# Performance work log

Measured on AMD Instinct MI355X. Metric: run time of the kernel, lower is better.

Reference implementation:

```python
import jax, jax.numpy as jnp
import numpy as np


def setup_inputs() -> dict:
    key = jax.random.key(0)
    k1, k2, k3, k4 = jax.random.split(key, 4)
    H = W = 1024
    B = 16
    image = jax.random.normal(k1, (1, H, W), dtype=jnp.float32)
    x = jax.random.normal(k2, (B, 1, H, W), dtype=jnp.float32)
    # Conv2d(1, 9, 3) parameters, torch layout: weight (out=9, in=1, 3, 3), bias (9,)
    fan_in = 1 * 3 * 3
    bound = 1.0 / np.sqrt(fan_in)
    W_KL = jax.random.uniform(k3, (9, 1, 3, 3), jnp.float32, -bound, bound)
    b_KL = jax.random.uniform(k4, (9,), jnp.float32, -bound, bound)
    return {"image": image, "x": x, "W_KL": W_KL, "b_KL": b_KL}


def reference(image, x, W_KL, b_KL):
    # K = Conv2d(image): (1,H,W) -> (9,H,W), 'same' padding
    K = jax.lax.conv_general_dilated(
        image[None], W_KL, window_strides=(1, 1), padding='SAME',
        dimension_numbers=('NCHW', 'OIHW', 'NCHW'))[0] + b_KL[:, None, None]
    H, W = image.shape[1], image.shape[2]
    # permute (9,H,W) -> (H,W,9) -> unflatten to per-pixel 3x3 kernels (H,W,3,3)
    K = jnp.transpose(K, (1, 2, 0)).reshape(H, W, 3, 3)
    # Apply spatially-varying 3x3 kernel: y[b,c,h,w] = sum_{a,d} K[h,w,a,d] * x_pad[b,c,h+a,w+d]
    x_pad = jnp.pad(x, ((0, 0), (0, 0), (1, 1), (1, 1)))
    y = jnp.zeros_like(x)
    for a in range(3):
        for d in range(3):
            y = y + K[:, :, a, d] * x_pad[:, :, a:a + H, d:d + W]
    return y
```

## Files before the change

kernel.cpp:

```cpp
#include <hip/hip_runtime.h>

#define IH 1024
#define IW 1024
#define NB 16

__global__ __launch_bounds__(512) void fused_smblock(
    const float* __restrict__ image,
    const float* __restrict__ x,
    const float* __restrict__ Wk,
    const float* __restrict__ bk,
    float* __restrict__ out)
{
    const int tx = threadIdx.x;
    const int ty = threadIdx.y;
    const int w0 = blockIdx.x * 256 + tx * 4;
    const int h  = blockIdx.y * 8 + ty;

    float wk[81];
#pragma unroll
    for (int i = 0; i < 81; ++i) wk[i] = Wk[i];
    float bb[9];
#pragma unroll
    for (int c = 0; c < 9; ++c) bb[c] = bk[c];

    float p[3][6];
#pragma unroll
    for (int a = 0; a < 3; ++a) {
        const int hh = h + a - 1;
        if (hh >= 0 && hh < IH) {
            const float* row = image + (size_t)hh * IW;
            p[a][0] = (w0 > 0) ? row[w0 - 1] : 0.f;
            const float4 m = *(const float4*)(row + w0);
            p[a][1] = m.x; p[a][2] = m.y; p[a][3] = m.z; p[a][4] = m.w;
            p[a][5] = (w0 + 4 < IW) ? row[w0 + 4] : 0.f;
        } else {
#pragma unroll
            for (int j = 0; j < 6; ++j) p[a][j] = 0.f;
        }
    }

    float Kv[4][9];
#pragma unroll
    for (int j = 0; j < 4; ++j) {
#pragma unroll
        for (int c = 0; c < 9; ++c) {
            float acc = bb[c];
#pragma unroll
            for (int i = 0; i < 3; ++i)
#pragma unroll
                for (int jj = 0; jj < 3; ++jj)
                    acc = fmaf(wk[c * 9 + i * 3 + jj], p[i][j + jj], acc);
            Kv[j][c] = acc;
        }
    }

    const size_t plane = (size_t)IH * IW;
#pragma unroll 2
    for (int b = 0; b < NB; ++b) {
        const float* xp = x + (size_t)b * plane;
        float r[3][6];
#pragma unroll
        for (int a = 0; a < 3; ++a) {
            const int hh = h + a - 1;
            if (hh >= 0 && hh < IH) {
                const float* row = xp + (size_t)hh * IW;
                r[a][0] = (w0 > 0) ? row[w0 - 1] : 0.f;
                const float4 m = *(const float4*)(row + w0);
                r[a][1] = m.x; r[a][2] = m.y; r[a][3] = m.z; r[a][4] = m.w;
                r[a][5] = (w0 + 4 < IW) ? row[w0 + 4] : 0.f;
            } else {
#pragma unroll
                for (int j = 0; j < 6; ++j) r[a][j] = 0.f;
            }
        }
        float yv[4];
#pragma unroll
        for (int j = 0; j < 4; ++j) {
            float acc = 0.f;
#pragma unroll
            for (int a = 0; a < 3; ++a)
#pragma unroll
                for (int d = 0; d < 3; ++d)
                    acc = fmaf(Kv[j][a * 3 + d], r[a][j + d], acc);
            yv[j] = acc;
        }
        *(float4*)(out + (size_t)b * plane + (size_t)h * IW + w0) =
            make_float4(yv[0], yv[1], yv[2], yv[3]);
    }
}

extern "C" void kernel_launch(void* const* d_in, const int* in_sizes, int n_in,
                              void* d_out, int out_size, void* d_ws, size_t ws_size,
                              hipStream_t stream) {
    const float* image = (const float*)d_in[0];
    const float* x     = (const float*)d_in[1];
    const float* Wk    = (const float*)d_in[2];
    const float* bk    = (const float*)d_in[3];
    float* out = (float*)d_out;

    dim3 block(64, 8);
    dim3 grid(IW / 256, IH / 8);
    fused_smblock<<<grid, block, 0, stream>>>(image, x, Wk, bk, out);
}
```

Measured before the change: 147.3 us.

## Split batch across grid z, use wave shuffles for halos, nontemporal stores

The batch loop is split across a third grid dimension so each block handles four batch planes instead of sixteen. This gives four times as many blocks to fill the GPU, at the cost of recomputing the per-pixel kernel from the image four times. Left and right halo values now come from neighbouring lanes through wave shuffles rather than separate scalar global loads, with only the wave-edge lanes still loading from memory. Output stores are marked nontemporal to reduce cache pollution from the streamed result.

```diff
diff --git a/kernel.cpp b/kernel.cpp
--- a/kernel.cpp
+++ b/kernel.cpp
@@ -3,6 +3,24 @@
 #define IH 1024
 #define IW 1024
 #define NB 16
+#define BPB 4
+
+typedef float v4f __attribute__((ext_vector_type(4)));
+
+__device__ __forceinline__ void load_row6(const float* __restrict__ row, int w0,
+                                          int tx, bool valid, float o[6]) {
+    if (valid) {
+        const v4f m = *(const v4f*)(row + w0);
+        float left  = __shfl_up(m.w, 1);
+        float right = __shfl_down(m.x, 1);
+        if (tx == 0)  left  = (w0 > 0)      ? row[w0 - 1] : 0.f;
+        if (tx == 63) right = (w0 + 4 < IW) ? row[w0 + 4] : 0.f;
+        o[0] = left; o[1] = m.x; o[2] = m.y; o[3] = m.z; o[4] = m.w; o[5] = right;
+    } else {
+#pragma unroll
+        for (int j = 0; j < 6; ++j) o[j] = 0.f;
+    }
+}
 
 __global__ __launch_bounds__(512) void fused_smblock(
     const float* __restrict__ image,
@@ -27,16 +45,8 @@
 #pragma unroll
     for (int a = 0; a < 3; ++a) {
         const int hh = h + a - 1;
-        if (hh >= 0 && hh < IH) {
-            const float* row = image + (size_t)hh * IW;
-            p[a][0] = (w0 > 0) ? row[w0 - 1] : 0.f;
-            const float4 m = *(const float4*)(row + w0);
-            p[a][1] = m.x; p[a][2] = m.y; p[a][3] = m.z; p[a][4] = m.w;
-            p[a][5] = (w0 + 4 < IW) ? row[w0 + 4] : 0.f;
-        } else {
-#pragma unroll
-            for (int j = 0; j < 6; ++j) p[a][j] = 0.f;
-        }
+        load_row6(image + (size_t)(hh < 0 ? 0 : hh) * IW, w0, tx,
+                  (hh >= 0 && hh < IH), p[a]);
     }
 
     float Kv[4][9];
@@ -55,23 +65,16 @@
     }
 
     const size_t plane = (size_t)IH * IW;
+    const int b0 = blockIdx.z * BPB;
 #pragma unroll 2
-    for (int b = 0; b < NB; ++b) {
-        const float* xp = x + (size_t)b * plane;
+    for (int bi = 0; bi < BPB; ++bi) {
+        const float* xp = x + (size_t)(b0 + bi) * plane;
         float r[3][6];
 #pragma unroll
         for (int a = 0; a < 3; ++a) {
             const int hh = h + a - 1;
-            if (hh >= 0 && hh < IH) {
-                const float* row = xp + (size_t)hh * IW;
-                r[a][0] = (w0 > 0) ? row[w0 - 1] : 0.f;
-                const float4 m = *(const float4*)(row + w0);
-                r[a][1] = m.x; r[a][2] = m.y; r[a][3] = m.z; r[a][4] = m.w;
-                r[a][5] = (w0 + 4 < IW) ? row[w0 + 4] : 0.f;
-            } else {
-#pragma unroll
-                for (int j = 0; j < 6; ++j) r[a][j] = 0.f;
-            }
+            load_row6(xp + (size_t)(hh < 0 ? 0 : hh) * IW, w0, tx,
+                      (hh >= 0 && hh < IH), r[a]);
         }
         float yv[4];
 #pragma unroll
@@ -84,8 +87,9 @@
                     acc = fmaf(Kv[j][a * 3 + d], r[a][j + d], acc);
             yv[j] = acc;
         }
-        *(float4*)(out + (size_t)b * plane + (size_t)h * IW + w0) =
-            make_float4(yv[0], yv[1], yv[2], yv[3]);
+        v4f yvec; yvec.x = yv[0]; yvec.y = yv[1]; yvec.z = yv[2]; yvec.w = yv[3];
+        __builtin_nontemporal_store(
+            yvec, (v4f*)(out + (size_t)(b0 + bi) * plane + (size_t)h * IW + w0));
     }
 }
 
@@ -99,6 +103,6 @@
     float* out = (float*)d_out;
 
     dim3 block(64, 8);
-    dim3 grid(IW / 256, IH / 8);
+    dim3 grid(IW / 256, IH / 8, NB / BPB);
     fused_smblock<<<grid, block, 0, stream>>>(image, x, Wk, bk, out);
 }
```

Result: no change. 148.0 us (+0.4%).

## Double-buffer batch window loads, use branchless vector loads and nontemporal stores

Applied to the files above, without the earlier changes.

Prefetches the 3x6 input window for the next batch plane into a second register buffer while computing the current one, so load latency overlaps with FMAs. Halo loads become branchless aligned float2/float4 loads with clamped addresses and select-based zeroing. Output stores use a nontemporal hint, and the block shrinks from 64x8 to 64x4 threads with launch bounds 256. The double buffer raises register pressure, which may cut occupancy, and the extra halo loads pull in more bytes per thread.

```diff
diff --git a/kernel.cpp b/kernel.cpp
--- a/kernel.cpp
+++ b/kernel.cpp
@@ -4,7 +4,31 @@
 #define IW 1024
 #define NB 16
 
-__global__ __launch_bounds__(512) void fused_smblock(
+typedef float v4f __attribute__((ext_vector_type(4)));
+typedef float v2f __attribute__((ext_vector_type(2)));
+
+__device__ __forceinline__ void load_win(const float* __restrict__ plane,
+                                         int h, int w0, float win[3][6]) {
+#pragma unroll
+    for (int a = 0; a < 3; ++a) {
+        const int hh = h + a - 1;
+        const bool rowok = (hh >= 0) & (hh < IH);
+        const float* rowp = plane + (size_t)(rowok ? hh : 0) * IW;
+        const v2f lv = *(const v2f*)(rowp + (w0 > 0 ? w0 - 2 : 0));
+        const v4f mv = *(const v4f*)(rowp + w0);
+        const v2f rv = *(const v2f*)(rowp + (w0 + 4 < IW ? w0 + 4 : IW - 2));
+        const float fl = (rowok && w0 > 0)       ? lv.y : 0.f;
+        const float fr = (rowok && w0 + 4 < IW)  ? rv.x : 0.f;
+        win[a][0] = fl;
+        win[a][1] = rowok ? mv.x : 0.f;
+        win[a][2] = rowok ? mv.y : 0.f;
+        win[a][3] = rowok ? mv.z : 0.f;
+        win[a][4] = rowok ? mv.w : 0.f;
+        win[a][5] = fr;
+    }
+}
+
+__global__ __launch_bounds__(256) void fused_smblock(
     const float* __restrict__ image,
     const float* __restrict__ x,
     const float* __restrict__ Wk,
@@ -14,7 +38,7 @@
     const int tx = threadIdx.x;
     const int ty = threadIdx.y;
     const int w0 = blockIdx.x * 256 + tx * 4;
-    const int h  = blockIdx.y * 8 + ty;
+    const int h  = blockIdx.y * 4 + ty;
 
     float wk[81];
 #pragma unroll
@@ -24,56 +48,32 @@
     for (int c = 0; c < 9; ++c) bb[c] = bk[c];
 
     float p[3][6];
-#pragma unroll
-    for (int a = 0; a < 3; ++a) {
-        const int hh = h + a - 1;
-        if (hh >= 0 && hh < IH) {
-            const float* row = image + (size_t)hh * IW;
-            p[a][0] = (w0 > 0) ? row[w0 - 1] : 0.f;
-            const float4 m = *(const float4*)(row + w0);
-            p[a][1] = m.x; p[a][2] = m.y; p[a][3] = m.z; p[a][4] = m.w;
-            p[a][5] = (w0 + 4 < IW) ? row[w0 + 4] : 0.f;
-        } else {
-#pragma unroll
-            for (int j = 0; j < 6; ++j) p[a][j] = 0.f;
-        }
-    }
-
+    load_win(image, h, w0, p);
     float Kv[4][9];
 #pragma unroll
-    for (int j = 0; j < 4; ++j) {
+    for (int j = 0; j < 4; ++j)
 #pragma unroll
         for (int c = 0; c < 9; ++c) {
             float acc = bb[c];
 #pragma unroll
-            for (int i = 0; i < 3; ++i)
+            for (int a = 0; a < 3; ++a)
 #pragma unroll
-                for (int jj = 0; jj < 3; ++jj)
-                    acc = fmaf(wk[c * 9 + i * 3 + jj], p[i][j + jj], acc);
+                for (int d = 0; d < 3; ++d)
+                    acc = fmaf(wk[c * 9 + a * 3 + d], p[a][j + d], acc);
             Kv[j][c] = acc;
         }
-    }
 
     const size_t plane = (size_t)IH * IW;
+    const size_t obase = (size_t)h * IW + w0;
+
+    float buf[2][3][6];
+    load_win(x, h, w0, buf[0]);
 #pragma unroll 2
     for (int b = 0; b < NB; ++b) {
-        const float* xp = x + (size_t)b * plane;
-        float r[3][6];
-#pragma unroll
-        for (int a = 0; a < 3; ++a) {
-            const int hh = h + a - 1;
-            if (hh >= 0 && hh < IH) {
-                const float* row = xp + (size_t)hh * IW;
-                r[a][0] = (w0 > 0) ? row[w0 - 1] : 0.f;
-                const float4 m = *(const float4*)(row + w0);
-                r[a][1] = m.x; r[a][2] = m.y; r[a][3] = m.z; r[a][4] = m.w;
-                r[a][5] = (w0 + 4 < IW) ? row[w0 + 4] : 0.f;
-            } else {
-#pragma unroll
-                for (int j = 0; j < 6; ++j) r[a][j] = 0.f;
-            }
-        }
-        float yv[4];
+        if (b + 1 < NB)
+            load_win(x + (size_t)(b + 1) * plane, h, w0, buf[(b + 1) & 1]);
+        const float (*r3)[6] = buf[b & 1];
+        v4f y;
 #pragma unroll
         for (int j = 0; j < 4; ++j) {
             float acc = 0.f;
@@ -81,11 +81,10 @@
             for (int a = 0; a < 3; ++a)
 #pragma unroll
                 for (int d = 0; d < 3; ++d)
-                    acc = fmaf(Kv[j][a * 3 + d], r[a][j + d], acc);
-            yv[j] = acc;
+                    acc = fmaf(Kv[j][a * 3 + d], r3[a][j + d], acc);
+            y[j] = acc;
         }
-        *(float4*)(out + (size_t)b * plane + (size_t)h * IW + w0) =
-            make_float4(yv[0], yv[1], yv[2], yv[3]);
+        __builtin_nontemporal_store(y, (v4f*)(out + (size_t)b * plane + obase));
     }
 }
 
@@ -98,7 +97,7 @@
     const float* bk    = (const float*)d_in[3];
     float* out = (float*)d_out;
 
-    dim3 block(64, 8);
-    dim3 grid(IW / 256, IH / 8);
+    dim3 block(64, 4);
+    dim3 grid(IW / 256, IH / 4);
     fused_smblock<<<grid, block, 0, stream>>>(image, x, Wk, bk, out);
 }
```

Result: faster. 138.9 us (-5.7%).
